# Performance work log

Measured on AMD Instinct MI355X. Metric: run time of the kernel, lower is better.

Reference implementation:

```python
import jax, jax.numpy as jnp
import numpy as np

# dims
N = 50000      # nodes
E = 400000     # edges
IN = 64        # in_channels
HID = 64       # hidden_channels (== GATConv out_channels)
H = 2          # heads
C = HID        # per-head out dim
L = 2          # num_layers
R = 4          # num_relations
EPS = 1e-5
NEG_SLOPE = 0.2


def setup_inputs() -> dict:
    key = jax.random.key(0)
    ks = jax.random.split(key, 10)
    x = jax.random.normal(ks[0], (N, IN), jnp.float32)
    edge_index = jax.random.randint(ks[1], (2, E), 0, N, jnp.int32)
    edge_weight = jax.random.normal(ks[2], (E,), jnp.float32)  # sign defines relation
    s_in = 1.0 / np.sqrt(IN)
    gat_W = jax.random.normal(ks[3], (L, R, IN, H * C), jnp.float32) * s_in
    gat_asrc = jax.random.normal(ks[4], (L, R, H, C), jnp.float32) * (1.0 / np.sqrt(C))
    gat_adst = jax.random.normal(ks[5], (L, R, H, C), jnp.float32) * (1.0 / np.sqrt(C))
    gat_bias = jnp.zeros((L, R, H * C), jnp.float32)
    mlp_in = IN + R * H * C
    mlp_W1 = jax.random.normal(ks[6], (L, mlp_in, HID), jnp.float32) / np.sqrt(mlp_in)
    mlp_b1 = jnp.zeros((L, HID), jnp.float32)
    mlp_W2 = jax.random.normal(ks[7], (L, HID, HID), jnp.float32) / np.sqrt(HID)
    mlp_b2 = jnp.zeros((L, HID), jnp.float32)
    ln_g = jnp.ones((L, HID), jnp.float32)
    ln_b = jnp.zeros((L, HID), jnp.float32)
    return dict(x=x, edge_index=edge_index, edge_weight=edge_weight,
                gat_W=gat_W, gat_asrc=gat_asrc, gat_adst=gat_adst, gat_bias=gat_bias,
                mlp_W1=mlp_W1, mlp_b1=mlp_b1, mlp_W2=mlp_W2, mlp_b2=mlp_b2,
                ln_g=ln_g, ln_b=ln_b)


def _gat(x, W, a_src, a_dst, bias, s, d, m):
    """PyG-style GATConv (source_to_target, self loops already in s/d, masked edges)."""
    h = (x @ W).reshape(-1, H, C)                  # [N,H,C]
    es = jnp.sum(h * a_src, axis=-1)               # [N,H] alpha_src per node
    ed = jnp.sum(h * a_dst, axis=-1)               # [N,H] alpha_dst per node
    e = jax.nn.leaky_relu(es[s] + ed[d], NEG_SLOPE)  # [Etot,H]
    e = jnp.where(m[:, None], e, -jnp.inf)
    emax = jax.ops.segment_max(e, d, num_segments=N)  # every node has a self loop
    p = jnp.exp(e - emax[d]) * m[:, None]
    den = jax.ops.segment_sum(p, d, num_segments=N)
    alpha = p / den[d]                             # segment softmax over incoming edges
    out = jax.ops.segment_sum(alpha[:, :, None] * h[s], d, num_segments=N)  # [N,H,C]
    return out.reshape(N, H * C) + bias


def reference(x, edge_index, edge_weight, gat_W, gat_asrc, gat_adst, gat_bias,
              mlp_W1, mlp_b1, mlp_W2, mlp_b2, ln_g, ln_b):
    src, dst = edge_index[0], edge_index[1]
    loop = jnp.arange(N, dtype=src.dtype)
    pos = edge_weight > 0
    neg = edge_weight < 0
    ones = jnp.ones((N,), bool)
    # relations: pos_out, pos_in (reversed), neg_out, neg_in (reversed); self loops always on
    rels = [
        (jnp.concatenate([src, loop]), jnp.concatenate([dst, loop]), jnp.concatenate([pos, ones])),
        (jnp.concatenate([dst, loop]), jnp.concatenate([src, loop]), jnp.concatenate([pos, ones])),
        (jnp.concatenate([src, loop]), jnp.concatenate([dst, loop]), jnp.concatenate([neg, ones])),
        (jnp.concatenate([dst, loop]), jnp.concatenate([src, loop]), jnp.concatenate([neg, ones])),
    ]
    h = x
    for l in range(L):
        feats = [_gat(h, gat_W[l, r], gat_asrc[l, r], gat_adst[l, r], gat_bias[l, r],
                      rels[r][0], rels[r][1], rels[r][2]) for r in range(R)]
        comb = jnp.concatenate([h] + feats, axis=1)          # [N, IN + 4*H*C]
        z = jnp.tanh(comb @ mlp_W1[l] + mlp_b1[l]) @ mlp_W2[l] + mlp_b2[l]
        z = z + h                                            # residual (IN == HID)
        mu = jnp.mean(z, axis=-1, keepdims=True)
        var = jnp.var(z, axis=-1, keepdims=True)
        h = (z - mu) / jnp.sqrt(var + EPS) * ln_g[l] + ln_b[l]
    return h
```

## Files before the change

kernel.cpp:

```cpp
#include <hip/hip_runtime.h>
#include <hip/hip_bf16.h>
#include <hip/hip_fp16.h>

typedef unsigned short u16;
typedef unsigned int u32;
typedef __attribute__((ext_vector_type(8))) short bf16x8;
typedef __attribute__((ext_vector_type(4))) float f32x4;

#define NODES 50000
#define NEDGE 400000
#define SCANN 200000
#define CAP 32
#define FOOTPRINT 138709280ull

__device__ __forceinline__ float bf2f(u16 u) { return __uint_as_float(((u32)u) << 16); }
__device__ __forceinline__ float bf2f_lo(u32 p) { return __uint_as_float(p << 16); }
__device__ __forceinline__ float bf2f_hi(u32 p) { return __uint_as_float(p & 0xffff0000u); }
__device__ __forceinline__ u16 f2bf(float f) {
    u32 u = __float_as_uint(f);
    u32 r = (u + 0x7fffu + ((u >> 16) & 1u)) >> 16;
    return (u16)r;
}
__device__ __forceinline__ u32 packbf2(float a, float b) {
    u32 ua = __float_as_uint(a) + 0x8000u;
    u32 ub = __float_as_uint(b) + 0x8000u;
    return __builtin_amdgcn_perm(ub, ua, 0x07060302u);
}
__device__ __forceinline__ float lrelu(float x) { return x > 0.f ? x : 0.2f * x; }

__device__ __forceinline__ float loadF(const void* p, long long i, int v) {
    if (v == 1) return ((const float*)p)[i];
    if (v == 2) return __half2float(((const __half*)p)[i]);
    return bf2f(((const u16*)p)[i]);
}
__device__ __forceinline__ int loadI(const void* p, long long i, int i64) {
    return i64 ? (int)((const long long*)p)[i] : ((const int*)p)[i];
}

__global__ void probe_k(const u16* __restrict__ x, int n,
                        const int* __restrict__ eidx, int* flag) {
    __shared__ int s0[256], s1[256];
    int t = threadIdx.x;
    if (blockIdx.x == 0) {
        int stride = n / 4096;
        int huge = 0, band = 0;
        for (int j = 0; j < 16; ++j) {
            int pos = (t * 16 + j) * stride;
            if (pos >= n) pos = n - 1;
            u32 e = ((u32)x[pos] >> 7) & 0xFF;
            huge += (e >= 0xC2) ? 1 : 0;
            band += (e >= 0x7A && e <= 0x81) ? 1 : 0;
        }
        s0[t] = huge; s1[t] = band;
        __syncthreads();
        if (t == 0) {
            int H = 0, B = 0;
            for (int i = 0; i < 256; ++i) { H += s0[i]; B += s1[i]; }
            int vF;
            if (H > 4) vF = 1;
            else if (B > 2048) vF = 0;
            else vF = 2;
            flag[0] = vF;
        }
    } else {
        int z = 0;
        for (int j = 0; j < 16; ++j) {
            int k = (t * 16 + j) * 97;
            z += (eidx[2 * k + 1] == 0) ? 1 : 0;
        }
        s0[t] = z;
        __syncthreads();
        if (t == 0) {
            int Z = 0;
            for (int i = 0; i < 256; ++i) Z += s0[i];
            flag[1] = (Z > 2048) ? 1 : 0;
            flag[2] = 0;
        }
    }
}

__global__ void decode_k(const void* asrc, const void* adst, const void* gatB,
                         const void* b1, const void* b2, const void* lng, const void* lnb,
                         const void* W1raw, const void* gWraw, const void* W2raw,
                         const void* xraw,
                         float* __restrict__ par, u16* __restrict__ w1p,
                         u16* __restrict__ wgp, u16* __restrict__ w2p,
                         int* __restrict__ cnt, float* __restrict__ h,
                         u16* __restrict__ hbf, const int* __restrict__ flag) {
    int vF = flag[0];
    if (blockIdx.x >= 782) {
        int i = (blockIdx.x - 782) * 256 + threadIdx.x;
        if (i >= NODES * 64) return;
        float v = loadF(xraw, i, vF);
        if (!isfinite(v)) v = 0.f;
        h[i] = v;
        hbf[i] = f2bf(v);
        return;
    }
    int i = blockIdx.x * 256 + threadIdx.x;
    if (i < SCANN) cnt[i] = 0;
    if (i >= 151040) return;
    if (i < 3584) {
        const void* src; int local;
        if      (i < 1024) { src = asrc; local = i; }
        else if (i < 2048) { src = adst; local = i - 1024; }
        else if (i < 3072) { src = gatB; local = i - 2048; }
        else if (i < 3200) { src = b1;   local = i - 3072; }
        else if (i < 3328) { src = b2;   local = i - 3200; }
        else if (i < 3456) { src = lng;  local = i - 3328; }
        else               { src = lnb;  local = i - 3456; }
        float v = loadF(src, local, vF);
        if (!isfinite(v)) v = 0.f;
        par[i] = v;
    } else if (i < 77312) {
        int id = i - 3584;
        int l = id / 36864;
        int rem = id % 36864;
        int ck = rem / 2048;
        int rem2 = rem % 2048;
        int ct = rem2 / 512;
        int rem3 = rem2 % 512;
        int lane = rem3 / 8;
        int j = rem3 % 8;
        float v = loadF(W1raw, (long long)l * 36864 +
                        (long long)(ck * 32 + (lane >> 4) * 8 + j) * 64 + ct * 16 + (lane & 15), vF);
        if (!isfinite(v)) v = 0.f;
        w1p[id] = f2bf(v);
    } else if (i < 142848) {
        int id = i - 77312;
        int lr = id / 8192;
        int rem = id % 8192;
        int ck = rem / 4096;
        int rem2 = rem % 4096;
        int ct = rem2 / 512;
        int rem3 = rem2 % 512;
        int lane = rem3 / 8;
        int j = rem3 % 8;
        float v = loadF(gWraw, (long long)lr * 8192 +
                        (long long)(ck * 32 + (lane >> 4) * 8 + j) * 128 + ct * 16 + (lane & 15), vF);
        if (!isfinite(v)) v = 0.f;
        wgp[id] = f2bf(v);
    } else {
        int id = i - 142848;
        int l = id / 4096;
        int rem = id % 4096;
        int ck = rem / 2048;
        int rem2 = rem % 2048;
        int ct = rem2 / 512;
        int rem3 = rem2 % 512;
        int lane = rem3 / 8;
        int j = rem3 % 8;
        float v = loadF(W2raw, (long long)l * 4096 +
                        (long long)(ck * 32 + (lane >> 4) * 8 + j) * 64 + ct * 16 + (lane & 15), vF);
        if (!isfinite(v)) v = 0.f;
        w2p[id] = f2bf(v);
    }
}

__global__ void scatter_k(const void* __restrict__ eidx, const void* __restrict__ ew,
                          int* __restrict__ cnt, u16* __restrict__ list, int e,
                          int* __restrict__ flag) {
    int i = blockIdx.x * 256 + threadIdx.x;
    if (i >= e) return;
    float w = loadF(ew, i, flag[0]);
    int base;
    if (w > 0.f) base = 0;
    else if (w < 0.f) base = 2;
    else return;
    int i64 = flag[1];
    int s = loadI(eidx, i, i64);
    int d = loadI(eidx, (long long)NEDGE + i, i64);
    if (s < 0 || s >= NODES || d < 0 || d >= NODES) return;
    int k = atomicAdd(&cnt[base * NODES + d], 1);
    if (k < CAP) list[((size_t)base * NODES + d) * CAP + k] = (u16)s;
    else atomicOr(&flag[2], 1);
    int k2 = atomicAdd(&cnt[(base + 1) * NODES + s], 1);
    if (k2 < CAP) list[((size_t)(base + 1) * NODES + s) * CAP + k2] = (u16)d;
    else atomicOr(&flag[2], 1);
}

__global__ __launch_bounds__(256) void hr4_mfma_k(const u16* __restrict__ hbf,
                                                  const u16* __restrict__ wgp,
                                                  u16* __restrict__ hr4,
                                                  const float* __restrict__ av,
                                                  const float* __restrict__ ad,
                                                  float* __restrict__ esed4, int nrows) {
    int r = blockIdx.y;
    int wave = threadIdx.x >> 6;
    int lane = threadIdx.x & 63;
    int q = lane >> 4, m = lane & 15;
    int row0 = blockIdx.x * 64 + wave * 16;
    int row = row0 + m;
    int rowc = (row < nrows) ? row : (nrows - 1);
    const bf16x8* wp = (const bf16x8*)(wgp + (size_t)r * 8192);
    u16* hr = hr4 + (size_t)r * NODES * 128;
    av += r * 128; ad += r * 128;
    float* esed = esed4 + (size_t)r * NODES * 4;

    f32x4 acc[8];
#pragma unroll
    for (int ct = 0; ct < 8; ++ct) acc[ct] = (f32x4){0.f, 0.f, 0.f, 0.f};
#pragma unroll
    for (int ck = 0; ck < 2; ++ck) {
        bf16x8 a = *(const bf16x8*)(hbf + (size_t)rowc * 64 + ck * 32 + q * 8);
#pragma unroll
        for (int ct = 0; ct < 8; ++ct) {
            bf16x8 b = wp[(ck * 8 + ct) * 64 + lane];
            acc[ct] = __builtin_amdgcn_mfma_f32_16x16x32_bf16(a, b, acc[ct], 0, 0, 0);
        }
    }
#pragma unroll
    for (int rr = 0; rr < 4; ++rr) {
        int ro = row0 + q * 4 + rr;
        if (ro >= nrows) continue;
        size_t base = (size_t)ro * 128;
#pragma unroll
        for (int ct = 0; ct < 8; ++ct) hr[base + ct * 16 + m] = f2bf(acc[ct][rr]);
    }
#pragma unroll
    for (int rr = 0; rr < 4; ++rr) {
        float e0 = 0.f, e1 = 0.f, d0 = 0.f, d1 = 0.f;
#pragma unroll
        for (int ct = 0; ct < 4; ++ct) {
            e0 += acc[ct][rr] * av[ct * 16 + m];
            d0 += acc[ct][rr] * ad[ct * 16 + m];
            e1 += acc[ct + 4][rr] * av[(ct + 4) * 16 + m];
            d1 += acc[ct + 4][rr] * ad[(ct + 4) * 16 + m];
        }
#pragma unroll
        for (int x = 1; x < 16; x <<= 1) {
            e0 += __shfl_xor(e0, x); e1 += __shfl_xor(e1, x);
            d0 += __shfl_xor(d0, x); d1 += __shfl_xor(d1, x);
        }
        int ro = row0 + q * 4 + rr;
        if (m == 0 && ro < nrows) {
            esed[ro * 4 + 0] = e0;
            esed[ro * 4 + 1] = e1;
            esed[ro * 4 + 2] = d0;
            esed[ro * 4 + 3] = d1;
        }
    }
}

__global__ __launch_bounds__(256) void mlp_ln_k(const u16* __restrict__ hbf,
                                                const u16* __restrict__ feat4,
                                                const u16* __restrict__ w1p,
                                                const float* __restrict__ b1,
                                                const u16* __restrict__ w2p,
                                                const float* __restrict__ b2,
                                                const float* __restrict__ hin,
                                                const float* __restrict__ g,
                                                const float* __restrict__ bsh,
                                                float* __restrict__ hout,
                                                u16* __restrict__ houtb,
                                                float* __restrict__ dout, int nrows) {
    __shared__ u16 st[4][16 * 72];
    int wave = threadIdx.x >> 6;
    int lane = threadIdx.x & 63;
    int q = lane >> 4, m = lane & 15;
    int row0 = blockIdx.x * 64 + wave * 16;
    int rowA = row0 + m;
    int rowc = (rowA < nrows) ? rowA : (nrows - 1);
    u16* my = st[wave];

    f32x4 acc0 = {0.f, 0.f, 0.f, 0.f};
    f32x4 acc1 = {0.f, 0.f, 0.f, 0.f};
    f32x4 acc2 = {0.f, 0.f, 0.f, 0.f};
    f32x4 acc3 = {0.f, 0.f, 0.f, 0.f};
    const bf16x8* wp = (const bf16x8*)w1p;
#pragma unroll
    for (int ck = 0; ck < 18; ++ck) {
        bf16x8 a;
        if (ck < 2) a = *(const bf16x8*)(hbf + (size_t)rowc * 64 + ck * 32 + q * 8);
        else        a = *(const bf16x8*)(feat4 + (size_t)rowc * 512 + (ck - 2) * 32 + q * 8);
        bf16x8 b0v = wp[(ck * 4 + 0) * 64 + lane];
        bf16x8 b1v = wp[(ck * 4 + 1) * 64 + lane];
        bf16x8 b2v = wp[(ck * 4 + 2) * 64 + lane];
        bf16x8 b3v = wp[(ck * 4 + 3) * 64 + lane];
        acc0 = __builtin_amdgcn_mfma_f32_16x16x32_bf16(a, b0v, acc0, 0, 0, 0);
        acc1 = __builtin_amdgcn_mfma_f32_16x16x32_bf16(a, b1v, acc1, 0, 0, 0);
        acc2 = __builtin_amdgcn_mfma_f32_16x16x32_bf16(a, b2v, acc2, 0, 0, 0);
        acc3 = __builtin_amdgcn_mfma_f32_16x16x32_bf16(a, b3v, acc3, 0, 0, 0);
    }
    float bv0 = b1[0 * 16 + m], bv1 = b1[1 * 16 + m], bv2 = b1[2 * 16 + m], bv3 = b1[3 * 16 + m];
#pragma unroll
    for (int rr = 0; rr < 4; ++rr) {
        int lr = q * 4 + rr;
        my[lr * 72 + 0 * 16 + m] = f2bf(tanhf(acc0[rr] + bv0));
        my[lr * 72 + 1 * 16 + m] = f2bf(tanhf(acc1[rr] + bv1));
        my[lr * 72 + 2 * 16 + m] = f2bf(tanhf(acc2[rr] + bv2));
        my[lr * 72 + 3 * 16 + m] = f2bf(tanhf(acc3[rr] + bv3));
    }
    f32x4 c0 = {0.f, 0.f, 0.f, 0.f};
    f32x4 c1 = {0.f, 0.f, 0.f, 0.f};
    f32x4 c2 = {0.f, 0.f, 0.f, 0.f};
    f32x4 c3 = {0.f, 0.f, 0.f, 0.f};
    const bf16x8* w2v = (const bf16x8*)w2p;
#pragma unroll
    for (int ck = 0; ck < 2; ++ck) {
        bf16x8 a = *(const bf16x8*)&my[m * 72 + ck * 32 + q * 8];
        c0 = __builtin_amdgcn_mfma_f32_16x16x32_bf16(a, w2v[(ck * 4 + 0) * 64 + lane], c0, 0, 0, 0);
        c1 = __builtin_amdgcn_mfma_f32_16x16x32_bf16(a, w2v[(ck * 4 + 1) * 64 + lane], c1, 0, 0, 0);
        c2 = __builtin_amdgcn_mfma_f32_16x16x32_bf16(a, w2v[(ck * 4 + 2) * 64 + lane], c2, 0, 0, 0);
        c3 = __builtin_amdgcn_mfma_f32_16x16x32_bf16(a, w2v[(ck * 4 + 3) * 64 + lane], c3, 0, 0, 0);
    }
    float b20 = b2[0 * 16 + m], b21 = b2[1 * 16 + m], b22 = b2[2 * 16 + m], b23 = b2[3 * 16 + m];
    float g0 = g[0 * 16 + m], g1 = g[1 * 16 + m], g2 = g[2 * 16 + m], g3 = g[3 * 16 + m];
    float s0 = bsh[0 * 16 + m], s1 = bsh[1 * 16 + m], s2 = bsh[2 * 16 + m], s3 = bsh[3 * 16 + m];
#pragma unroll
    for (int rr = 0; rr < 4; ++rr) {
        int ro = row0 + q * 4 + rr;
        int roc = (ro < nrows) ? ro : (nrows - 1);
        size_t base = (size_t)roc * 64;
        float v0 = c0[rr] + b20 + hin[base + 0 * 16 + m];
        float v1 = c1[rr] + b21 + hin[base + 1 * 16 + m];
        float v2 = c2[rr] + b22 + hin[base + 2 * 16 + m];
        float v3 = c3[rr] + b23 + hin[base + 3 * 16 + m];
        float s = v0 + v1 + v2 + v3;
#pragma unroll
        for (int x = 1; x < 16; x <<= 1) s += __shfl_xor(s, x);
        float mu = s * (1.f / 64.f);
        float qv = (v0 - mu) * (v0 - mu) + (v1 - mu) * (v1 - mu) +
                   (v2 - mu) * (v2 - mu) + (v3 - mu) * (v3 - mu);
#pragma unroll
        for (int x = 1; x < 16; x <<= 1) qv += __shfl_xor(qv, x);
        float rstd = rsqrtf(qv * (1.f / 64.f) + 1e-5f);
        float o0 = (v0 - mu) * rstd * g0 + s0;
        float o1 = (v1 - mu) * rstd * g1 + s1;
        float o2 = (v2 - mu) * rstd * g2 + s2;
        float o3 = (v3 - mu) * rstd * g3 + s3;
        if (ro < nrows) {
            hout[base + 0 * 16 + m] = o0;
            hout[base + 1 * 16 + m] = o1;
            hout[base + 2 * 16 + m] = o2;
            hout[base + 3 * 16 + m] = o3;
            houtb[base + 0 * 16 + m] = f2bf(o0);
            houtb[base + 1 * 16 + m] = f2bf(o1);
            houtb[base + 2 * 16 + m] = f2bf(o2);
            houtb[base + 3 * 16 + m] = f2bf(o3);
            if (dout) {
                dout[base + 0 * 16 + m] = o0;
                dout[base + 1 * 16 + m] = o1;
                dout[base + 2 * 16 + m] = o2;
                dout[base + 3 * 16 + m] = o3;
            }
        }
    }
}

__global__ __launch_bounds__(256) void agg4_k(const u16* __restrict__ hr4,
                                              const float* __restrict__ esed4,
                                              const int* __restrict__ cnt,
                                              const u16* __restrict__ list,
                                              const float* __restrict__ gatB_l,
                                              u16* __restrict__ feat4, int n) {
    int wave = threadIdx.x >> 6;
    int lane = threadIdx.x & 63;
    int g = lane >> 4;
    int L = lane & 15;
    int head = L >> 3;
    int node = blockIdx.x * 16 + wave * 4 + g;
    int r = blockIdx.y;
    const uint4* hrv = (const uint4*)(hr4 + (size_t)r * NODES * 128);
    const float* esed = esed4 + (size_t)r * NODES * 4;
    const float* bias = gatB_l + r * 128;

    bool valid = node < n;
    int nodec = valid ? node : 0;
    float myed = esed[nodec * 4 + 2 + head];
    float p = __expf(lrelu(esed[nodec * 4 + head] + myed));
    uint4 v = hrv[nodec * 16 + L];
    float a0 = p * bf2f_lo(v.x), a1 = p * bf2f_hi(v.x);
    float a2 = p * bf2f_lo(v.y), a3 = p * bf2f_hi(v.y);
    float a4 = p * bf2f_lo(v.z), a5 = p * bf2f_hi(v.z);
    float a6 = p * bf2f_lo(v.w), a7 = p * bf2f_hi(v.w);
    float den = p;
    int deg = valid ? cnt[r * NODES + nodec] : 0;
    if (deg > CAP) deg = CAP;
    const u16* mylist = list + ((size_t)r * NODES + nodec) * CAP;
    int nb = (deg > 0) ? (int)mylist[0] : 0;
    for (int j = 0; j < deg; ++j) {
        int nbn = (j + 1 < deg) ? (int)mylist[j + 1] : 0;
        float2 es2 = *(const float2*)(esed + nb * 4);
        uint4 vv = hrv[nb * 16 + L];
        float pe = __expf(lrelu((head ? es2.y : es2.x) + myed));
        a0 += pe * bf2f_lo(vv.x); a1 += pe * bf2f_hi(vv.x);
        a2 += pe * bf2f_lo(vv.y); a3 += pe * bf2f_hi(vv.y);
        a4 += pe * bf2f_lo(vv.z); a5 += pe * bf2f_hi(vv.z);
        a6 += pe * bf2f_lo(vv.w); a7 += pe * bf2f_hi(vv.w);
        den += pe;
        nb = nbn;
    }
    if (valid) {
        float inv = 1.f / den;
        const float* bb = bias + 8 * L;
        u32 o0 = packbf2(a0 * inv + bb[0], a1 * inv + bb[1]);
        u32 o1 = packbf2(a2 * inv + bb[2], a3 * inv + bb[3]);
        u32 o2 = packbf2(a4 * inv + bb[4], a5 * inv + bb[5]);
        u32 o3 = packbf2(a6 * inv + bb[6], a7 * inv + bb[7]);
        uint4* fp = (uint4*)feat4;
        fp[node * 64 + r * 16 + L] = make_uint4(o0, o1, o2, o3);
    }
}

__global__ void beacon_k(const int* __restrict__ flag, const float* __restrict__ lng,
                         int hostcode, int ws_ok, float* __restrict__ out) {
    if (blockIdx.x != 0 || threadIdx.x != 0) return;
    if (flag[2]) out[0] = 5000.f;
    float mx = 0.f;
    for (int c = 0; c < 64; ++c) {
        float d = fabsf(lng[c] - 1.f);
        if (d > mx) mx = d;
    }
    if (mx > 0.01f) out[0] = 6000.f;
    if (hostcode) out[0] = (float)hostcode;
    if (!ws_ok) out[0] = 9000.f;
}

extern "C" void kernel_launch(void* const* d_in, const int* in_sizes, int n_in,
                              void* d_out, int out_size, void* d_ws, size_t ws_size,
                              hipStream_t stream) {
    const void* eidx = d_in[1];
    float* out = (float*)d_out;

    char* ws = (char*)d_ws;
    float* h     = (float*)(ws + 0);
    u16*   hbf   = (u16*)(ws + 12800000);
    u16*   hr4   = (u16*)(ws + 19200000);
    u16*   feat4 = (u16*)(ws + 70400000);
    float* esed4 = (float*)(ws + 121600000);
    int* cnt     = (int*)(ws + 124800000);
    u16* list    = (u16*)(ws + 125600000);
    float* par   = (float*)(ws + 138400000);
    u16*   wgp   = (u16*)(ws + 138414336);
    u16*   w1p   = (u16*)(ws + 138545408);
    u16*   w2p   = (u16*)(ws + 138692864);
    int*   flag  = (int*)(ws + 138709248);

    float* asrc_f = par;
    float* adst_f = par + 1024;
    float* gatB_f = par + 2048;
    float* b1_f   = par + 3072;
    float* b2_f   = par + 3200;
    float* lng_f  = par + 3328;
    float* lnb_f  = par + 3456;

    int ws_ok = (ws_size >= FOOTPRINT) ? 1 : 0;
    int hostcode = 0;
    {
        const int expect[13] = {3200000, 800000, 400000, 65536, 1024, 1024, 1024,
                                73728, 128, 8192, 128, 128, 128};
        if (n_in != 13 || out_size != 3200000) hostcode = 11000;
        else {
            for (int i = 0; i < 13; ++i)
                if (in_sizes[i] != expect[i]) { hostcode = 10000 + 50 * i; break; }
        }
    }

    probe_k<<<2, 256, 0, stream>>>((const u16*)d_in[0], NODES * 64, (const int*)eidx, flag);
    decode_k<<<782 + (NODES * 64 + 255) / 256, 256, 0, stream>>>(
        d_in[4], d_in[5], d_in[6], d_in[8], d_in[10], d_in[11], d_in[12],
        d_in[7], d_in[3], d_in[9], d_in[0],
        par, w1p, wgp, w2p, cnt, h, hbf, flag);

    scatter_k<<<(NEDGE + 255) / 256, 256, 0, stream>>>(eidx, d_in[2], cnt, list, NEDGE, flag);

    for (int l = 0; l < 2; ++l) {
        hr4_mfma_k<<<dim3((NODES + 63) / 64, 4), 256, 0, stream>>>(
            hbf, wgp + (size_t)l * 32768, hr4,
            asrc_f + l * 512, adst_f + l * 512, esed4, NODES);
        agg4_k<<<dim3((NODES + 15) / 16, 4), 256, 0, stream>>>(
            hr4, esed4, cnt, list, gatB_f + l * 512, feat4, NODES);
        mlp_ln_k<<<(NODES + 63) / 64, 256, 0, stream>>>(
            hbf, feat4, w1p + (size_t)l * 36864, b1_f + l * 64,
            w2p + (size_t)l * 4096, b2_f + l * 64,
            h, lng_f + l * 64, lnb_f + l * 64, h, hbf,
            (l == 1) ? out : nullptr, NODES);
    }
    beacon_k<<<1, 64, 0, stream>>>(flag, lng_f, hostcode, ws_ok, out);
}
```

Baseline: 367.8 us.

## Fold edge scatter into decode and first GAT projection kernels

Removes the standalone scatter kernel and splits the edge-list build in two. The first half of the edges is scattered by extra blocks appended to the decode kernel, and the second half by an extra grid row in the layer-0 projection kernel. Counter zeroing moves from the decode kernel to a hipMemsetAsync. This cuts one launch and lets the atomic-heavy scatter overlap with decode and GEMM work, at the cost of a memset and some extra divergence and grid size in those kernels.

```diff
diff --git a/kernel.cpp b/kernel.cpp
--- a/kernel.cpp
+++ b/kernel.cpp
@@ -9,7 +9,6 @@
 
 #define NODES 50000
 #define NEDGE 400000
-#define SCANN 200000
 #define CAP 32
 #define FOOTPRINT 138709280ull
 
@@ -35,6 +34,27 @@
 }
 __device__ __forceinline__ int loadI(const void* p, long long i, int i64) {
     return i64 ? (int)((const long long*)p)[i] : ((const int*)p)[i];
+}
+
+__device__ __forceinline__ void scatter_edge(const void* __restrict__ eidx,
+                                             const void* __restrict__ ew,
+                                             int* __restrict__ cnt, u16* __restrict__ list,
+                                             int* __restrict__ flag, int i) {
+    float w = loadF(ew, i, flag[0]);
+    int base;
+    if (w > 0.f) base = 0;
+    else if (w < 0.f) base = 2;
+    else return;
+    int i64 = flag[1];
+    int s = loadI(eidx, i, i64);
+    int d = loadI(eidx, (long long)NEDGE + i, i64);
+    if (s < 0 || s >= NODES || d < 0 || d >= NODES) return;
+    int k = atomicAdd(&cnt[base * NODES + d], 1);
+    if (k < CAP) list[((size_t)base * NODES + d) * CAP + k] = (u16)s;
+    else atomicOr(&flag[2], 1);
+    int k2 = atomicAdd(&cnt[(base + 1) * NODES + s], 1);
+    if (k2 < CAP) list[((size_t)(base + 1) * NODES + s) * CAP + k2] = (u16)d;
+    else atomicOr(&flag[2], 1);
 }
 
 __global__ void probe_k(const u16* __restrict__ x, int n,
@@ -82,12 +102,18 @@
 __global__ void decode_k(const void* asrc, const void* adst, const void* gatB,
                          const void* b1, const void* b2, const void* lng, const void* lnb,
                          const void* W1raw, const void* gWraw, const void* W2raw,
-                         const void* xraw,
+                         const void* xraw, const void* eidx, const void* ew,
                          float* __restrict__ par, u16* __restrict__ w1p,
                          u16* __restrict__ wgp, u16* __restrict__ w2p,
-                         int* __restrict__ cnt, float* __restrict__ h,
-                         u16* __restrict__ hbf, const int* __restrict__ flag) {
+                         int* __restrict__ cnt, u16* __restrict__ list,
+                         float* __restrict__ h, u16* __restrict__ hbf,
+                         int* __restrict__ flag) {
     int vF = flag[0];
+    if (blockIdx.x >= 13282) {
+        int i = (blockIdx.x - 13282) * 256 + threadIdx.x;
+        if (i < NEDGE / 2) scatter_edge(eidx, ew, cnt, list, flag, i);
+        return;
+    }
     if (blockIdx.x >= 782) {
         int i = (blockIdx.x - 782) * 256 + threadIdx.x;
         if (i >= NODES * 64) return;
@@ -98,7 +124,6 @@
         return;
     }
     int i = blockIdx.x * 256 + threadIdx.x;
-    if (i < SCANN) cnt[i] = 0;
     if (i >= 151040) return;
     if (i < 3584) {
         const void* src; int local;
@@ -157,35 +182,23 @@
     }
 }
 
-__global__ void scatter_k(const void* __restrict__ eidx, const void* __restrict__ ew,
-                          int* __restrict__ cnt, u16* __restrict__ list, int e,
-                          int* __restrict__ flag) {
-    int i = blockIdx.x * 256 + threadIdx.x;
-    if (i >= e) return;
-    float w = loadF(ew, i, flag[0]);
-    int base;
-    if (w > 0.f) base = 0;
-    else if (w < 0.f) base = 2;
-    else return;
-    int i64 = flag[1];
-    int s = loadI(eidx, i, i64);
-    int d = loadI(eidx, (long long)NEDGE + i, i64);
-    if (s < 0 || s >= NODES || d < 0 || d >= NODES) return;
-    int k = atomicAdd(&cnt[base * NODES + d], 1);
-    if (k < CAP) list[((size_t)base * NODES + d) * CAP + k] = (u16)s;
-    else atomicOr(&flag[2], 1);
-    int k2 = atomicAdd(&cnt[(base + 1) * NODES + s], 1);
-    if (k2 < CAP) list[((size_t)(base + 1) * NODES + s) * CAP + k2] = (u16)d;
-    else atomicOr(&flag[2], 1);
-}
-
 __global__ __launch_bounds__(256) void hr4_mfma_k(const u16* __restrict__ hbf,
                                                   const u16* __restrict__ wgp,
                                                   u16* __restrict__ hr4,
                                                   const float* __restrict__ av,
                                                   const float* __restrict__ ad,
-                                                  float* __restrict__ esed4, int nrows) {
+                                                  float* __restrict__ esed4, int nrows,
+                                                  const void* __restrict__ eidx,
+                                                  const void* __restrict__ ew,
+                                                  int* __restrict__ cnt,
+                                                  u16* __restrict__ list,
+                                                  int* __restrict__ flag) {
     int r = blockIdx.y;
+    if (r == 4) {
+        int i = NEDGE / 2 + blockIdx.x * 256 + threadIdx.x;
+        if (i < NEDGE) scatter_edge(eidx, ew, cnt, list, flag, i);
+        return;
+    }
     int wave = threadIdx.x >> 6;
     int lane = threadIdx.x & 63;
     int q = lane >> 4, m = lane & 15;
@@ -457,18 +470,19 @@
         }
     }
 
+    hipMemsetAsync(cnt, 0, 4 * NODES * sizeof(int), stream);
     probe_k<<<2, 256, 0, stream>>>((const u16*)d_in[0], NODES * 64, (const int*)eidx, flag);
-    decode_k<<<782 + (NODES * 64 + 255) / 256, 256, 0, stream>>>(
+
+    decode_k<<<13282 + 782, 256, 0, stream>>>(
         d_in[4], d_in[5], d_in[6], d_in[8], d_in[10], d_in[11], d_in[12],
-        d_in[7], d_in[3], d_in[9], d_in[0],
-        par, w1p, wgp, w2p, cnt, h, hbf, flag);
-
-    scatter_k<<<(NEDGE + 255) / 256, 256, 0, stream>>>(eidx, d_in[2], cnt, list, NEDGE, flag);
+        d_in[7], d_in[3], d_in[9], d_in[0], eidx, d_in[2],
+        par, w1p, wgp, w2p, cnt, list, h, hbf, flag);
 
     for (int l = 0; l < 2; ++l) {
-        hr4_mfma_k<<<dim3((NODES + 63) / 64, 4), 256, 0, stream>>>(
+        hr4_mfma_k<<<dim3((NODES + 63) / 64, (l == 0) ? 5 : 4), 256, 0, stream>>>(
             hbf, wgp + (size_t)l * 32768, hr4,
-            asrc_f + l * 512, adst_f + l * 512, esed4, NODES);
+            asrc_f + l * 512, adst_f + l * 512, esed4, NODES,
+            eidx, d_in[2], cnt, list, flag);
         agg4_k<<<dim3((NODES + 15) / 16, 4), 256, 0, stream>>>(
             hr4, esed4, cnt, list, gatB_f + l * 512, feat4, NODES);
         mlp_ln_k<<<(NODES + 63) / 64, 256, 0, stream>>>(
```

Measured after the change: 362.2 us. No clear change (-1.5%).
